# Optimization experiments

Measured on AMD Instinct MI355X. Metric: run time of the kernel, lower is better.

Reference implementation:

```python
import jax, jax.numpy as jnp
import numpy as np

INPUT_DIM = 66
OUTPUT_COUNT = 8192
NUM_PAIRS = 65536

def setup_inputs() -> dict:
    key = jax.random.key(0)
    k1, k2, k3, k4 = jax.random.split(key, 4)
    x = jax.random.normal(k1, (NUM_PAIRS, INPUT_DIM), dtype=jnp.float32)
    query = jax.random.normal(k2, (OUTPUT_COUNT, INPUT_DIM), dtype=jnp.float32)
    # nn.Linear(input_dim, input_dim): weight [out,in], bias [out]
    bound = 1.0 / np.sqrt(INPUT_DIM)
    Wk = jax.random.uniform(k3, (INPUT_DIM, INPUT_DIM), minval=-bound, maxval=bound, dtype=jnp.float32)
    bk = jax.random.uniform(k4, (INPUT_DIM,), minval=-bound, maxval=bound, dtype=jnp.float32)
    return {"x": x, "query": query, "Wk": Wk, "bk": bk}

def reference(x, query, Wk, bk):
    # K = Linear(x): x @ Wk^T + bk  -> [num_pairs, d]
    K = x @ Wk.T + bk
    # scores: [output_count, num_pairs]
    scores = jnp.einsum("qd,nd->qn", query, K)
    attn = jax.nn.softmax(scores, axis=1)
    # selected: [output_count, d] — note values are raw x, not K
    selected = attn @ x
    return selected
```

## Files before the change

### kernel.cpp

```cpp
#include <hip/hip_runtime.h>
#include <cstdint>


typedef __bf16    bf16x4 __attribute__((ext_vector_type(4)));
typedef __bf16    bf16x8 __attribute__((ext_vector_type(8)));
typedef _Float16  f16x4  __attribute__((ext_vector_type(4)));
typedef _Float16  f16x8  __attribute__((ext_vector_type(8)));
typedef float     f32x2  __attribute__((ext_vector_type(2)));
typedef float     f32x16 __attribute__((ext_vector_type(16)));

extern "C" __device__ float __ocml_native_exp2_f32(float);

#define NUM_PAIRS   65536
#define NUM_Q       8192
#define DIM         66
#define QPITCH      80
#define KFT         2560
#define XFT         3072
#define PARTP       68
#define NS          16
#define NTILES      (NUM_PAIRS/32)

#define XBYTES      6144
#define CHUNK_X     (2*XBYTES)

__device__ __forceinline__ f32x16 mfma_bf16(bf16x8 a, bf16x8 b, f32x16 c) {
    return __builtin_amdgcn_mfma_f32_32x32x16_bf16(a, b, c, 0, 0, 0);
}
__device__ __forceinline__ f32x16 mfma_f16(f16x8 a, f16x8 b, f32x16 c) {
    return __builtin_amdgcn_mfma_f32_32x32x16_f16(a, b, c, 0, 0, 0);
}
__device__ __forceinline__ void plswap(unsigned &a, unsigned &b) {
    asm volatile("s_nop 1\n\t"
                 "v_permlane32_swap_b32 %0, %1\n\t"
                 "s_nop 1"
                 : "+v"(a), "+v"(b));
}
__device__ __forceinline__ unsigned packbf(float a, float b) {
    union { __bf16 h[2]; unsigned u; } t;
    t.h[0] = (__bf16)a; t.h[1] = (__bf16)b;
    return t.u;
}
union U4 { unsigned u[4]; bf16x8 v; };

__device__ __forceinline__ void gload16(const void* g, void* l) {
    __builtin_amdgcn_global_load_lds(
        (const __attribute__((address_space(1))) unsigned int*)g,
        (__attribute__((address_space(3))) unsigned int*)l,
        16, 0, 0);
}

__device__ __forceinline__ void makefrags(const f32x16 &s, U4 *f) {
    float P[16];
    #pragma unroll
    for (int r = 0; r < 16; ++r) P[r] = __ocml_native_exp2_f32(s[r]);
    unsigned E0 = packbf(P[0],  P[1]),  E1 = packbf(P[2],  P[3]);
    unsigned F0 = packbf(P[4],  P[5]),  F1 = packbf(P[6],  P[7]);
    plswap(E0, F0); plswap(E1, F1);
    f[0].u[0] = E0; f[0].u[1] = E1; f[0].u[2] = F0; f[0].u[3] = F1;
    unsigned G0 = packbf(P[8],  P[9]),  G1 = packbf(P[10], P[11]);
    unsigned H0 = packbf(P[12], P[13]), H1 = packbf(P[14], P[15]);
    plswap(G0, H0); plswap(G1, H1);
    f[1].u[0] = G0; f[1].u[1] = G1; f[1].u[2] = H0; f[1].u[3] = H1;
}

#define PAP 104
__global__ __launch_bounds__(256) void prep_kernel(
    const float* __restrict__ x, const float* __restrict__ query,
    const float* __restrict__ Wk,
    unsigned short* __restrict__ Af_u, unsigned short* __restrict__ Xf_u,
    unsigned short* __restrict__ Qh_u) {
    const int tid = threadIdx.x;
    const int lane = tid & 63, w = tid >> 6;
    const int l31 = lane & 31, h = lane >> 5;

    if (blockIdx.x >= 512) {
        __shared__ _Float16 sq[128 * PAP];
        __shared__ _Float16 sWT[96 * PAP];
        _Float16* Qh = (_Float16*)Qh_u;
        const long q0 = (long)(blockIdx.x - 512) * 128;

        for (int i = tid; i < 128 * PAP / 2; i += 256) ((unsigned*)sq)[i] = 0u;
        for (int i = tid; i < 96 * PAP / 2; i += 256)  ((unsigned*)sWT)[i] = 0u;
        __syncthreads();

        for (int i = tid; i < 128 * 33; i += 256) {
            int r = i / 33, c2 = (i % 33) * 2;
            f32x2 v = *(const f32x2*)&query[(q0 + r) * DIM + c2];
            sq[r * PAP + c2]     = (_Float16)v.x;
            sq[r * PAP + c2 + 1] = (_Float16)v.y;
        }
        for (int i = tid; i < DIM * 33; i += 256) {
            int d = i / 33, e2 = (i % 33) * 2;
            f32x2 v = *(const f32x2*)&Wk[d * DIM + e2];
            sWT[e2 * PAP + d]       = (_Float16)(v.x * 1.4426950408889634f);
            sWT[(e2 + 1) * PAP + d] = (_Float16)(v.y * 1.4426950408889634f);
        }
        __syncthreads();

        #pragma unroll
        for (int nt = 0; nt < 3; ++nt) {
            f32x16 acc = {};
            #pragma unroll
            for (int kk = 0; kk < 6; ++kk) {
                f16x8 a = *(const f16x8*)&sq[(w * 32 + l31) * PAP + kk * 16 + h * 8];
                f16x8 b = *(const f16x8*)&sWT[(nt * 32 + l31) * PAP + kk * 16 + h * 8];
                acc = mfma_f16(a, b, acc);
            }
            int c = nt * 32 + l31;
            if (c < QPITCH) {
                #pragma unroll
                for (int r = 0; r < 16; ++r) {
                    int row = (r & 3) + 8 * (r >> 2) + 4 * h;
                    Qh[(q0 + w * 32 + row) * QPITCH + c] = (_Float16)acc[r];
                }
            }
        }
        return;
    }

    _Float16* Af = (_Float16*)Af_u;
    __bf16*   Xf = (__bf16*)Xf_u;
    __shared__ _Float16 sxh[128 * PAP];
    const long n0 = (long)blockIdx.x * 128;

    for (int i = tid; i < 128 * PAP / 2; i += 256) ((unsigned*)sxh)[i] = 0u;
    __syncthreads();
    for (int i = tid; i < 128 * 33; i += 256) {
        int r = i / 33, c2 = (i % 33) * 2;
        f32x2 v = *(const f32x2*)&x[(n0 + r) * DIM + c2];
        sxh[r * PAP + c2]     = (_Float16)v.x;
        sxh[r * PAP + c2 + 1] = (_Float16)v.y;
    }
    for (int r = tid; r < 128; r += 256) sxh[r * PAP + DIM] = (_Float16)1.0f;
    __syncthreads();

    for (int i = 0; i < 5; ++i) {
        int slot = i * 256 + tid;
        int tt = slot / 320, rem = slot % 320;
        int kk = rem / 64, l = rem % 64;
        const _Float16* src = &sxh[(32 * tt + (l & 31)) * PAP + kk * 16 + (l >> 5) * 8];
        f16x4 lo = *(const f16x4*)src;
        f16x4 hi = *(const f16x4*)(src + 4);
        f16x8 v = __builtin_shufflevector(lo, hi, 0, 1, 2, 3, 4, 5, 6, 7);
        *(f16x8*)&Af[((long)blockIdx.x * 4 + tt) * KFT + kk * 512 + l * 8] = v;
    }
    for (int i = 0; i < 6; ++i) {
        int slot = i * 256 + tid;
        int tt = slot / 384, rem = slot % 384;
        int c = rem / 64, l = rem % 64;
        int dt = c % 3, par = c / 3;
        int d = 32 * dt + (l & 31);
        int p0 = 32 * tt + 16 * par + 8 * (l >> 5);
        bf16x8 v;
        #pragma unroll
        for (int j = 0; j < 8; ++j)
            v[j] = (__bf16)(float)sxh[(p0 + j) * PAP + d];
        *(bf16x8*)&Xf[((long)blockIdx.x * 4 + tt) * XFT + c * 512 + l * 8] = v;
    }
}

__global__ __launch_bounds__(256, 2) void flash_kernel(
    const unsigned short* __restrict__ Qh_u, const unsigned short* __restrict__ Af_u,
    const unsigned short* __restrict__ Xf_u, unsigned short* __restrict__ Part_u) {
    const _Float16* Qh = (const _Float16*)Qh_u;
    const _Float16* Af = (const _Float16*)Af_u;
    const __bf16*   Xf = (const __bf16*)Xf_u;
    __bf16* Part = (__bf16*)Part_u;

    const int tid = threadIdx.x;
    const int lane = tid & 63, wave = tid >> 6;
    const int l31 = lane & 31, h = lane >> 5;
    const int qb = blockIdx.x / NS, ns = blockIdx.x % NS;
    const int tiles = NTILES / NS;
    const int nchunks = tiles / 2;
    const int qbase = qb * 256 + wave * 64;

    const _Float16* kf = Af + (long)(ns * tiles) * KFT + lane * 8;
    const char*     Xg = (const char*)(Xf + (long)(ns * tiles) * XFT);

    __shared__ __align__(16) char smem[2 * CHUNK_X];

    auto stageX = [&](int m, int pb) {
        char* b = smem + pb * CHUNK_X;
        const char* g = Xg + (long)(2 * m) * XBYTES;
        #pragma unroll
        for (int r = 0; r < 3; ++r)
            gload16(g + r * 4096 + tid * 16, b + r * 4096 + tid * 16);
    };

    f16x8 aQ[2][5];
    #pragma unroll
    for (int qt = 0; qt < 2; ++qt)
        #pragma unroll
        for (int kk = 0; kk < 5; ++kk)
            aQ[qt][kk] = *(const f16x8*)&Qh[(long)(qbase + qt * 32 + l31) * QPITCH + kk * 16 + h * 8];

    f32x16 o[2][3] = {};
    f16x8  kA[5], kB[5];
    f32x16 s0, s1;

    stageX(0, 0);
    #pragma unroll
    for (int kk = 0; kk < 5; ++kk) kA[kk] = *(const f16x8*)(kf + kk * 512);
    #pragma unroll
    for (int kk = 0; kk < 5; ++kk) kB[kk] = *(const f16x8*)(kf + KFT + kk * 512);
    {
        f32x16 a = {}, b = {};
        #pragma unroll
        for (int kk = 0; kk < 5; ++kk) {
            a = mfma_f16(kA[kk], aQ[0][kk], a);
            b = mfma_f16(kA[kk], aQ[1][kk], b);
        }
        s0 = a; s1 = b;
    }
    __syncthreads();

    auto tilestep = [&](int t, const char* xbase, f16x8 (&kPre)[5],
                        const f16x8 (&kNext)[5]) {
        {
            long tk = (t + 2 < tiles) ? (long)(t + 2) : (long)(tiles - 1);
            const _Float16* kp = kf + tk * KFT;
            #pragma unroll
            for (int kk = 0; kk < 5; ++kk) kPre[kk] = *(const f16x8*)(kp + kk * 512);
        }
        bf16x8 xR[6];
        #pragma unroll
        for (int cc = 0; cc < 6; ++cc)
            xR[cc] = *(const bf16x8*)(xbase + cc * 1024 + lane * 16);

        U4 f0[2];
        makefrags(s0, f0);
        {
            f32x16 nsv = {};
            #pragma unroll
            for (int kk = 0; kk < 5; ++kk) nsv = mfma_f16(kNext[kk], aQ[0][kk], nsv);
            s0 = nsv;
        }
        #pragma unroll
        for (int par = 0; par < 2; ++par)
            #pragma unroll
            for (int dt = 0; dt < 3; ++dt)
                o[0][dt] = mfma_bf16(f0[par].v, xR[par * 3 + dt], o[0][dt]);

        U4 f1[2];
        makefrags(s1, f1);
        {
            f32x16 nsv = {};
            #pragma unroll
            for (int kk = 0; kk < 5; ++kk) nsv = mfma_f16(kNext[kk], aQ[1][kk], nsv);
            s1 = nsv;
        }
        #pragma unroll
        for (int par = 0; par < 2; ++par)
            #pragma unroll
            for (int dt = 0; dt < 3; ++dt)
                o[1][dt] = mfma_bf16(f1[par].v, xR[par * 3 + dt], o[1][dt]);
    };

    for (int c = 0; c < nchunks; ++c) {
        if (c + 1 < nchunks) stageX(c + 1, (c + 1) & 1);
        const char* bX = smem + (c & 1) * CHUNK_X;
        tilestep(2 * c,     bX,          kA, kB);
        tilestep(2 * c + 1, bX + XBYTES, kB, kA);
        __syncthreads();
    }

    #pragma unroll
    for (int qt = 0; qt < 2; ++qt)
        #pragma unroll
        for (int dt = 0; dt < 3; ++dt)
            #pragma unroll
            for (int r = 0; r < 16; ++r) {
                int row = (r & 3) + 8 * (r >> 2) + 4 * h;
                int q = qbase + qt * 32 + row;
                int d = dt * 32 + l31;
                if (d < DIM + 1)
                    Part[((long)q * NS + ns) * PARTP + d] = (__bf16)o[qt][dt][r];
            }
}

__global__ __launch_bounds__(256) void combine_kernel(
    const unsigned short* __restrict__ Part_u, float* __restrict__ out) {
    const __bf16* Part = (const __bf16*)Part_u;
    int q = blockIdx.x * 2 + (threadIdx.x >> 7);
    int d = threadIdx.x & 127;
    if (d >= DIM) return;
    const __bf16* base = Part + (long)q * NS * PARTP;
    float num = 0.f, den = 0.f;
    #pragma unroll 4
    for (int s = 0; s < NS; ++s) {
        num += (float)base[s * PARTP + d];
        den += (float)base[s * PARTP + DIM];
    }
    out[(long)q * DIM + d] = num / den;
}

extern "C" void kernel_launch(void* const* d_in, const int* in_sizes, int n_in,
                              void* d_out, int out_size, void* d_ws, size_t ws_size,
                              hipStream_t stream) {
    const float* x     = (const float*)d_in[0];
    const float* query = (const float*)d_in[1];
    const float* Wk    = (const float*)d_in[2];
    float* out = (float*)d_out;
    char* ws = (char*)d_ws;

    unsigned short* Qh   = (unsigned short*)(ws + 0);
    unsigned short* Af   = (unsigned short*)(ws + 1310720);
    unsigned short* Xf   = (unsigned short*)(ws + 11796480);
    unsigned short* Part = (unsigned short*)(ws + 24379392);

    prep_kernel<<<512 + NUM_Q / 128, 256, 0, stream>>>(x, query, Wk, Af, Xf, Qh);
    flash_kernel<<<(NUM_Q / 256) * NS, 256, 0, stream>>>(Qh, Af, Xf, Part);
    combine_kernel<<<NUM_Q / 2, 256, 0, stream>>>(Part, out);
}
```

Before: 261.3 us.

## Stage K tiles through LDS and shrink per-wave query tile for higher occupancy

```diff
diff --git a/kernel.cpp b/kernel.cpp
--- a/kernel.cpp
+++ b/kernel.cpp
@@ -21,8 +21,9 @@
 #define NS          16
 #define NTILES      (NUM_PAIRS/32)
 
-#define XBYTES      6144
-#define CHUNK_X     (2*XBYTES)
+#define TILE_K_B    5120
+#define TILE_X_B    6144
+#define CH_B        (TILE_K_B+TILE_X_B)
 
 __device__ __forceinline__ f32x16 mfma_bf16(bf16x8 a, bf16x8 b, f32x16 c) {
     return __builtin_amdgcn_mfma_f32_32x32x16_bf16(a, b, c, 0, 0, 0);
@@ -160,7 +161,7 @@
     }
 }
 
-__global__ __launch_bounds__(256, 2) void flash_kernel(
+__global__ __launch_bounds__(256, 4) void flash_kernel(
     const unsigned short* __restrict__ Qh_u, const unsigned short* __restrict__ Af_u,
     const unsigned short* __restrict__ Xf_u, unsigned short* __restrict__ Part_u) {
     const _Float16* Qh = (const _Float16*)Qh_u;
@@ -173,111 +174,88 @@
     const int l31 = lane & 31, h = lane >> 5;
     const int qb = blockIdx.x / NS, ns = blockIdx.x % NS;
     const int tiles = NTILES / NS;
-    const int nchunks = tiles / 2;
-    const int qbase = qb * 256 + wave * 64;
-
-    const _Float16* kf = Af + (long)(ns * tiles) * KFT + lane * 8;
-    const char*     Xg = (const char*)(Xf + (long)(ns * tiles) * XFT);
-
-    __shared__ __align__(16) char smem[2 * CHUNK_X];
-
-    auto stageX = [&](int m, int pb) {
-        char* b = smem + pb * CHUNK_X;
-        const char* g = Xg + (long)(2 * m) * XBYTES;
-        #pragma unroll
-        for (int r = 0; r < 3; ++r)
-            gload16(g + r * 4096 + tid * 16, b + r * 4096 + tid * 16);
+    const int qbase = qb * 128 + wave * 32;
+
+    const char* Kg = (const char*)(Af + (long)(ns * tiles) * KFT);
+    const char* Xg = (const char*)(Xf + (long)(ns * tiles) * XFT);
+
+    __shared__ __align__(16) char smem[2 * CH_B];
+
+    auto stage = [&](int t, int pb) {
+        char* bK = smem + pb * CH_B;
+        char* bX = bK + TILE_K_B;
+        long ka = (t + 1 < tiles) ? (long)(t + 1) : (long)(tiles - 1);
+        long xa = (long)t;
+        gload16(Kg + ka * TILE_K_B + tid * 16, bK + tid * 16);
+        if (tid < 64)
+            gload16(Kg + ka * TILE_K_B + 4096 + tid * 16, bK + 4096 + tid * 16);
+        gload16(Xg + xa * TILE_X_B + tid * 16, bX + tid * 16);
+        if (tid < 128)
+            gload16(Xg + xa * TILE_X_B + 4096 + tid * 16, bX + 4096 + tid * 16);
     };
 
-    f16x8 aQ[2][5];
+    f16x8 aQ[5];
     #pragma unroll
-    for (int qt = 0; qt < 2; ++qt)
+    for (int kk = 0; kk < 5; ++kk)
+        aQ[kk] = *(const f16x8*)&Qh[(long)(qbase + l31) * QPITCH + kk * 16 + h * 8];
+
+    f32x16 o[3] = {};
+    f32x16 s0;
+
+    stage(0, 0);
+    {
+        const _Float16* kf = Af + (long)(ns * tiles) * KFT + lane * 8;
+        f16x8 kA[5];
+        #pragma unroll
+        for (int kk = 0; kk < 5; ++kk) kA[kk] = *(const f16x8*)(kf + kk * 512);
+        f32x16 a = {};
+        #pragma unroll
+        for (int kk = 0; kk < 5; ++kk) a = mfma_f16(kA[kk], aQ[kk], a);
+        s0 = a;
+    }
+    __syncthreads();
+
+    for (int t = 0; t < tiles; ++t) {
+        if (t + 1 < tiles) stage(t + 1, (t + 1) & 1);
+        const char* bK = smem + (t & 1) * CH_B;
+        const char* bX = bK + TILE_K_B;
+
+        f16x8 kR[5];
         #pragma unroll
         for (int kk = 0; kk < 5; ++kk)
-            aQ[qt][kk] = *(const f16x8*)&Qh[(long)(qbase + qt * 32 + l31) * QPITCH + kk * 16 + h * 8];
-
-    f32x16 o[2][3] = {};
-    f16x8  kA[5], kB[5];
-    f32x16 s0, s1;
-
-    stageX(0, 0);
-    #pragma unroll
-    for (int kk = 0; kk < 5; ++kk) kA[kk] = *(const f16x8*)(kf + kk * 512);
-    #pragma unroll
-    for (int kk = 0; kk < 5; ++kk) kB[kk] = *(const f16x8*)(kf + KFT + kk * 512);
-    {
-        f32x16 a = {}, b = {};
-        #pragma unroll
-        for (int kk = 0; kk < 5; ++kk) {
-            a = mfma_f16(kA[kk], aQ[0][kk], a);
-            b = mfma_f16(kA[kk], aQ[1][kk], b);
-        }
-        s0 = a; s1 = b;
-    }
-    __syncthreads();
-
-    auto tilestep = [&](int t, const char* xbase, f16x8 (&kPre)[5],
-                        const f16x8 (&kNext)[5]) {
-        {
-            long tk = (t + 2 < tiles) ? (long)(t + 2) : (long)(tiles - 1);
-            const _Float16* kp = kf + tk * KFT;
-            #pragma unroll
-            for (int kk = 0; kk < 5; ++kk) kPre[kk] = *(const f16x8*)(kp + kk * 512);
-        }
+            kR[kk] = *(const f16x8*)(bK + kk * 1024 + lane * 16);
         bf16x8 xR[6];
         #pragma unroll
         for (int cc = 0; cc < 6; ++cc)
-            xR[cc] = *(const bf16x8*)(xbase + cc * 1024 + lane * 16);
+            xR[cc] = *(const bf16x8*)(bX + cc * 1024 + lane * 16);
 
         U4 f0[2];
         makefrags(s0, f0);
         {
             f32x16 nsv = {};
             #pragma unroll
-            for (int kk = 0; kk < 5; ++kk) nsv = mfma_f16(kNext[kk], aQ[0][kk], nsv);
+            for (int kk = 0; kk < 5; ++kk) nsv = mfma_f16(kR[kk], aQ[kk], nsv);
             s0 = nsv;
         }
         #pragma unroll
         for (int par = 0; par < 2; ++par)
             #pragma unroll
             for (int dt = 0; dt < 3; ++dt)
-                o[0][dt] = mfma_bf16(f0[par].v, xR[par * 3 + dt], o[0][dt]);
-
-        U4 f1[2];
-        makefrags(s1, f1);
-        {
-            f32x16 nsv = {};
-            #pragma unroll
-            for (int kk = 0; kk < 5; ++kk) nsv = mfma_f16(kNext[kk], aQ[1][kk], nsv);
-            s1 = nsv;
-        }
-        #pragma unroll
-        for (int par = 0; par < 2; ++par)
-            #pragma unroll
-            for (int dt = 0; dt < 3; ++dt)
-                o[1][dt] = mfma_bf16(f1[par].v, xR[par * 3 + dt], o[1][dt]);
-    };
-
-    for (int c = 0; c < nchunks; ++c) {
-        if (c + 1 < nchunks) stageX(c + 1, (c + 1) & 1);
-        const char* bX = smem + (c & 1) * CHUNK_X;
-        tilestep(2 * c,     bX,          kA, kB);
-        tilestep(2 * c + 1, bX + XBYTES, kB, kA);
+                o[dt] = mfma_bf16(f0[par].v, xR[par * 3 + dt], o[dt]);
+
         __syncthreads();
     }
 
     #pragma unroll
-    for (int qt = 0; qt < 2; ++qt)
-        #pragma unroll
-        for (int dt = 0; dt < 3; ++dt)
-            #pragma unroll
-            for (int r = 0; r < 16; ++r) {
-                int row = (r & 3) + 8 * (r >> 2) + 4 * h;
-                int q = qbase + qt * 32 + row;
-                int d = dt * 32 + l31;
-                if (d < DIM + 1)
-                    Part[((long)q * NS + ns) * PARTP + d] = (__bf16)o[qt][dt][r];
-            }
+    for (int dt = 0; dt < 3; ++dt)
+        #pragma unroll
+        for (int r = 0; r < 16; ++r) {
+            int row = (r & 3) + 8 * (r >> 2) + 4 * h;
+            int q = qbase + row;
+            int d = dt * 32 + l31;
+            if (d < DIM + 1)
+                Part[((long)q * NS + ns) * PARTP + d] = (__bf16)o[dt][r];
+        }
 }
 
 __global__ __launch_bounds__(256) void combine_kernel(
@@ -311,6 +289,6 @@
     unsigned short* Part = (unsigned short*)(ws + 24379392);
 
     prep_kernel<<<512 + NUM_Q / 128, 256, 0, stream>>>(x, query, Wk, Af, Xf, Qh);
-    flash_kernel<<<(NUM_Q / 256) * NS, 256, 0, stream>>>(Qh, Af, Xf, Part);
+    flash_kernel<<<(NUM_Q / 128) * NS, 256, 0, stream>>>(Qh, Af, Xf, Part);
     combine_kernel<<<NUM_Q / 2, 256, 0, stream>>>(Part, out);
 }
```

Result: slower. 281.8 us (+7.8%).
